# Kernel optimization log

Measured on AMD Instinct MI355X. Metric: run time of the kernel, lower is better.

## Reference

```python
import jax, jax.numpy as jnp
import numpy as np
from jax import lax

NUM_MASK_PARAMS = 67  # 66 weights (64 feat + 2 coord channels) + 1 bias
NUM_GEN_PARAMS = 134


def _coord_maps(h, w, dtype):
    yy = jnp.broadcast_to(jnp.linspace(-1.0, 1.0, h, dtype=dtype)[:, None], (h, w))
    xx = jnp.broadcast_to(jnp.linspace(-1.0, 1.0, w, dtype=dtype)[None, :], (h, w))
    return xx, yy


def _dynamic_head(x_cat, p):
    # x_cat: [66, H, W]; p: [num_ins, 67] -> [num_ins, H, W]
    w = p[:, :NUM_MASK_PARAMS - 1]
    b = p[:, NUM_MASK_PARAMS - 1]
    return jnp.einsum('ic,chw->ihw', w, x_cat) + b[:, None, None]


def setup_inputs() -> dict:
    key = jax.random.key(0)
    ks = jax.random.split(key, 10)
    C, HM, WM, HH, WH, MB, HID = 256, 272, 480, 136, 240, 64, 64
    rn = lambda k, s, sc=1.0: jax.random.normal(k, s, dtype=jnp.float32) * sc
    return {
        'out0': rn(ks[0], (1, C, HM, WM)),
        'out1': rn(ks[1], (1, C, HH, WH)),
        'hm_w': rn(ks[2], (1, C), 0.05),
        'hm_b': jnp.zeros((1,), jnp.float32),
        'params_w': rn(ks[3], (NUM_GEN_PARAMS, C), 0.05),
        'params_b': rn(ks[4], (NUM_GEN_PARAMS,), 0.05),
        'mb_w': rn(ks[5], (MB, C, 3, 3), 0.05),
        'mb_b': jnp.zeros((MB,), jnp.float32),
        'mlp_w1': rn(ks[6], (HM, HID), 0.05),
        'mlp_b1': jnp.zeros((HID,), jnp.float32),
        'mlp_w2': rn(ks[7], (HID, 2), 0.05),
        'mlp_b2': jnp.zeros((2,), jnp.float32),
        'num_ins': 4,
    }


def reference(out0, out1, hm_w, hm_b, params_w, params_b, mb_w, mb_b,
              mlp_w1, mlp_b1, mlp_w2, mlp_b2, num_ins):
    h_mask, w_mask = out0.shape[2], out0.shape[3]
    h_hm, w_hm = out1.shape[2], out1.shape[3]

    # ctnet head: 1x1 convs on the stride-16 feature
    hm = jnp.einsum('kc,bchw->bkhw', hm_w, out1) + hm_b[None, :, None, None]
    params = jnp.einsum('kc,bchw->bkhw', params_w, out1) + params_b[None, :, None, None]
    hm = jnp.clip(jax.nn.sigmoid(hm), 1e-4, 1.0 - 1e-4)  # [1,1,h_hm,w_hm]
    # [1,134,h,w] -> [h*w, 134]
    params_flat = jnp.transpose(params[0], (1, 2, 0)).reshape(-1, NUM_GEN_PARAMS)

    # 3x3 maxpool NMS (stride 1, pad 1), keep only local peaks
    hmax = lax.reduce_window(hm, -jnp.inf, lax.max, (1, 1, 3, 3), (1, 1, 1, 1),
                             [(0, 0), (0, 0), (1, 1), (1, 1)])
    keep = (hmax == hm).astype(hm.dtype)
    heat_nms = (hm * keep).reshape(-1)

    scores, inds = lax.top_k(heat_nms, num_ins)

    # mask branch: 3x3 conv + relu on the stride-8 feature
    mask_branch = lax.conv_general_dilated(out0, mb_w, (1, 1), 'SAME',
                                           dimension_numbers=('NCHW', 'OIHW', 'NCHW'))
    mask_branch = jax.nn.relu(mask_branch + mb_b[None, :, None, None])  # [1,64,H,W]

    xx, yy = _coord_maps(h_mask, w_mask, mask_branch.dtype)
    x_cat = jnp.concatenate([mask_branch[0], xx[None], yy[None]], axis=0)  # [66,H,W]

    gen_params = params_flat[inds]  # [num_ins, 134]
    masks0 = _dynamic_head(x_cat, gen_params[:, :NUM_MASK_PARAMS])   # [num_ins,H,W]
    regs0 = _dynamic_head(x_cat, gen_params[:, NUM_MASK_PARAMS:])    # [num_ins,H,W]

    # row-wise vertical-range MLP over h_mask
    feat_range = jnp.transpose(masks0, (0, 2, 1))  # [num_ins, w_mask, h_mask]
    h1 = jax.nn.relu(feat_range @ mlp_w1 + mlp_b1)
    feat_range = h1 @ mlp_w2 + mlp_b2  # [num_ins, w_mask, 2]

    return scores, inds, regs0, masks0, feat_range
```

## Files before the change

kernel.cpp:

```cpp
#include <hip/hip_runtime.h>
#include <math.h>
#include <limits.h>

#define C_IN 256
#define HM_H 136
#define HM_W 240
#define HM_N (HM_H * HM_W)
#define MB   64
#define MH   272
#define MW   480
#define MN   (MH * MW)
#define NP   134
#define NI   4
#define HID  64

#define REG_OFF   8
#define MASK_OFF  (8 + NI * MN)
#define FEAT_OFF  (8 + 2 * NI * MN)

#define WS_HM   0
#define WS_CV   HM_N
#define WS_CI   (HM_N + 512)
#define WS_GP   (2 * HM_N)
#define WS_INDS (2 * HM_N + NI * NP)
#define WS_WT_F 65824

typedef float  f32x4  __attribute__((ext_vector_type(4)));
typedef short  bf16x8 __attribute__((ext_vector_type(8)));

__device__ __forceinline__ unsigned short f2bf(float f) {
  unsigned int u = __float_as_uint(f);
  u += 0x7FFFu + ((u >> 16) & 1u);
  return (unsigned short)(u >> 16);
}
__device__ __forceinline__ float b2f(unsigned short h) {
  return __uint_as_float(((unsigned int)h) << 16);
}

__global__ void k_wprep(const float* __restrict__ mb_w, unsigned short* __restrict__ wt) {
  int idx = blockIdx.x * 256 + threadIdx.x;
  int j    = idx & 7;
  int lane = (idx >> 3) & 63;
  int nt   = (idx >> 9) & 3;
  int gt   = idx >> 11;
  int t    = gt % 9;
  int g    = gt / 9;
  int n = nt * 16 + (lane & 15);
  int c = g * 32 + (lane >> 4) * 8 + j;
  wt[idx] = f2bf(mb_w[(n * C_IN + c) * 9 + t]);
}

__global__ void k_hm(const float* __restrict__ out1, const float* __restrict__ hm_w,
                     const float* __restrict__ hm_b, float* __restrict__ ws_hm) {
  __shared__ float part[4][64];
  int b = blockIdx.x, t = threadIdx.x;
  int cg = t >> 6, pl = t & 63;
  int p = b * 64 + pl;
  float s = 0.f;
  #pragma unroll 16
  for (int c = 0; c < 64; ++c)
    s += hm_w[cg * 64 + c] * out1[(cg * 64 + c) * HM_N + p];
  part[cg][pl] = s;
  __syncthreads();
  if (t < 64) {
    float tot = part[0][t] + part[1][t] + part[2][t] + part[3][t] + hm_b[0];
    float sig = 1.f / (1.f + expf(-tot));
    sig = fminf(fmaxf(sig, 1e-4f), 1.f - 1e-4f);
    ws_hm[b * 64 + t] = sig;
  }
}

__device__ __forceinline__ bool better(float av, int ai, float bv, int bi) {
  return (av > bv) || (av == bv && ai < bi);
}

template<int NTHR>
__device__ void top4_tree(float* sv, int* si, int t) {
  for (int s = NTHR / 2; s >= 1; s >>= 1) {
    if (t < s) {
      float a[4], b[4]; int ai[4], bj[4];
      #pragma unroll
      for (int k = 0; k < 4; ++k) {
        a[k] = sv[t * 4 + k];        ai[k] = si[t * 4 + k];
        b[k] = sv[(t + s) * 4 + k];  bj[k] = si[(t + s) * 4 + k];
      }
      float ov[4]; int oi[4];
      int i = 0, j = 0;
      #pragma unroll
      for (int k = 0; k < 4; ++k) {
        if (better(a[i], ai[i], b[j], bj[j])) { ov[k] = a[i]; oi[k] = ai[i]; ++i; }
        else                                   { ov[k] = b[j]; oi[k] = bj[j]; ++j; }
      }
      #pragma unroll
      for (int k = 0; k < 4; ++k) { sv[t * 4 + k] = ov[k]; si[t * 4 + k] = oi[k]; }
    }
    __syncthreads();
  }
}

__global__ void k_nms_top(const float* __restrict__ ws_hm, float* __restrict__ candv,
                          int* __restrict__ candi) {
  __shared__ float sv[256 * 4];
  __shared__ int   si[256 * 4];
  int b = blockIdx.x, t = threadIdx.x;
  float v = -1.f; int idx = INT_MAX;
  if (t < 255) {
    int p = b * 255 + t;
    int y = p / HM_W, x = p - y * HM_W;
    float c = ws_hm[p], m = c;
    #pragma unroll
    for (int dy = -1; dy <= 1; ++dy)
      #pragma unroll
      for (int dx = -1; dx <= 1; ++dx) {
        int yy = y + dy, xx = x + dx;
        if (yy >= 0 && yy < HM_H && xx >= 0 && xx < HM_W)
          m = fmaxf(m, ws_hm[yy * HM_W + xx]);
      }
    v = (c == m) ? c : 0.f;
    idx = p;
  }
  sv[t * 4] = v; si[t * 4] = idx;
  #pragma unroll
  for (int k = 1; k < 4; ++k) { sv[t * 4 + k] = -1.f; si[t * 4 + k] = INT_MAX; }
  __syncthreads();
  top4_tree<256>(sv, si, t);
  if (t == 0) {
    #pragma unroll
    for (int k = 0; k < 4; ++k) { candv[b * 4 + k] = sv[k]; candi[b * 4 + k] = si[k]; }
  }
}

__global__ void k_topk_final(const float* __restrict__ candv, const int* __restrict__ candi,
                             int* __restrict__ ws_inds, float* __restrict__ d_out) {
  __shared__ float sv[128 * 4];
  __shared__ int   si[128 * 4];
  int t = threadIdx.x;
  #pragma unroll
  for (int k = 0; k < 4; ++k) { sv[t * 4 + k] = candv[t * 4 + k]; si[t * 4 + k] = candi[t * 4 + k]; }
  __syncthreads();
  top4_tree<128>(sv, si, t);
  if (t == 0) {
    #pragma unroll
    for (int k = 0; k < 4; ++k) {
      d_out[k]     = sv[k];
      d_out[4 + k] = (float)si[k];
      ws_inds[k]   = si[k];
    }
  }
}

__global__ void k_gen(const float* __restrict__ out1, const float* __restrict__ params_w,
                      const float* __restrict__ params_b, const int* __restrict__ ws_inds,
                      float* __restrict__ ws_gp) {
  __shared__ float col[C_IN];
  int i = blockIdx.x;
  int p = ws_inds[i];
  col[threadIdx.x] = out1[threadIdx.x * HM_N + p];
  __syncthreads();
  int j = threadIdx.x;
  if (j < NP) {
    float s = params_b[j];
    #pragma unroll 8
    for (int c = 0; c < C_IN; ++c) s += params_w[j * C_IN + c] * col[c];
    ws_gp[i * NP + j] = s;
  }
}

#define CS 40
#define RP 36
#define BUFU 14400

__global__ __launch_bounds__(256, 2) void k_conv_mfma(
    const float* __restrict__ out0, const unsigned short* __restrict__ wt,
    const float* __restrict__ mb_b, const float* __restrict__ ws_gp,
    float* __restrict__ d_out) {
  __shared__ unsigned short smem[2 * BUFU];

  int tid  = threadIdx.x;
  int lane = tid & 63;
  int w    = tid >> 6;
  int n15  = lane & 15;
  int kq   = lane >> 4;
  int gx0 = blockIdx.x * 32, gy0 = blockIdx.y * 8;

  int goff[25], lofs[25];
  unsigned int mld = 0, mst0 = 0, mst1 = 0;
  #pragma unroll
  for (int i = 0; i < 25; ++i) {
    int u = tid + 256 * i;
    int c   = u / 200;
    int rem = u - c * 200;
    int row = rem / 20;
    int q   = rem - row * 20;
    int iy  = gy0 + row - 1;
    int ixe = gx0 + 2 * q - 2;
    bool vld = (iy >= 0) && (iy < MH) && (ixe >= 0) && (ixe < MW);
    goff[i] = vld ? (c * MN + iy * MW + ixe) : 0;
    if (vld) mld |= (1u << i);
    int x0 = 2 * q - 1;
    lofs[i] = (row * RP + x0) * CS + c;
    if (x0 >= 0 && x0 < RP)     mst0 |= (1u << i);
    if (x0 + 1 < RP)            mst1 |= (1u << i);
  }

  int rrow[4], xbas[4];
  #pragma unroll
  for (int i = 0; i < 4; ++i) {
    int mt = w * 4 + i;
    rrow[i] = mt >> 1;
    xbas[i] = (mt & 1) * 16 + n15;
  }

  {
    float2 d[25];
    #pragma unroll
    for (int i = 0; i < 25; ++i) d[i] = *(const float2*)(out0 + goff[i]);
    #pragma unroll
    for (int i = 0; i < 25; ++i) {
      bool vl = (mld >> i) & 1;
      float a = vl ? d[i].x : 0.f, bb = vl ? d[i].y : 0.f;
      if ((mst0 >> i) & 1) smem[lofs[i]]      = f2bf(a);
      if ((mst1 >> i) & 1) smem[lofs[i] + CS] = f2bf(bb);
    }
  }
  __syncthreads();

  f32x4 acc[4][4];
  #pragma unroll
  for (int i = 0; i < 4; ++i)
    #pragma unroll
    for (int nt = 0; nt < 4; ++nt)
      acc[i][nt] = (f32x4){0.f, 0.f, 0.f, 0.f};

  #pragma unroll 1
  for (int g = 0; g < 8; ++g) {
    const unsigned short* cur = smem + (g & 1) * BUFU;
    unsigned short*       nxt = smem + ((g + 1) & 1) * BUFU;
    const float*          src = out0 + (g + 1) * (32 * MN);
    float2 d[25];

    if (g < 7) {
      #pragma unroll
      for (int i = 0; i < 13; ++i) d[i] = *(const float2*)(src + goff[i]);
    }
    #pragma unroll
    for (int t = 0; t < 4; ++t) {
      int ty = t / 3, tx = t - ty * 3;
      const unsigned short* wb = wt + (g * 9 + t) * 2048 + lane * 8;
      bf16x8 bfrag[4], afrag[4];
      #pragma unroll
      for (int nt = 0; nt < 4; ++nt) bfrag[nt] = *(const bf16x8*)(wb + nt * 512);
      #pragma unroll
      for (int i = 0; i < 4; ++i)
        afrag[i] = *(const bf16x8*)&cur[((rrow[i] + ty) * RP + xbas[i] + tx) * CS + kq * 8];
      #pragma unroll
      for (int i = 0; i < 4; ++i)
        #pragma unroll
        for (int nt = 0; nt < 4; ++nt)
          acc[i][nt] = __builtin_amdgcn_mfma_f32_16x16x32_bf16(afrag[i], bfrag[nt], acc[i][nt], 0, 0, 0);
    }
    if (g < 7) {
      #pragma unroll
      for (int i = 0; i < 13; ++i) {
        bool vl = (mld >> i) & 1;
        float a = vl ? d[i].x : 0.f, bb = vl ? d[i].y : 0.f;
        if ((mst0 >> i) & 1) nxt[lofs[i]]      = f2bf(a);
        if ((mst1 >> i) & 1) nxt[lofs[i] + CS] = f2bf(bb);
      }
      #pragma unroll
      for (int i = 13; i < 25; ++i) d[i] = *(const float2*)(src + goff[i]);
    }
    #pragma unroll
    for (int t = 4; t < 9; ++t) {
      int ty = t / 3, tx = t - ty * 3;
      const unsigned short* wb = wt + (g * 9 + t) * 2048 + lane * 8;
      bf16x8 bfrag[4], afrag[4];
      #pragma unroll
      for (int nt = 0; nt < 4; ++nt) bfrag[nt] = *(const bf16x8*)(wb + nt * 512);
      #pragma unroll
      for (int i = 0; i < 4; ++i)
        afrag[i] = *(const bf16x8*)&cur[((rrow[i] + ty) * RP + xbas[i] + tx) * CS + kq * 8];
      #pragma unroll
      for (int i = 0; i < 4; ++i)
        #pragma unroll
        for (int nt = 0; nt < 4; ++nt)
          acc[i][nt] = __builtin_amdgcn_mfma_f32_16x16x32_bf16(afrag[i], bfrag[nt], acc[i][nt], 0, 0, 0);
    }
    if (g < 7) {
      #pragma unroll
      for (int i = 13; i < 25; ++i) {
        bool vl = (mld >> i) & 1;
        float a = vl ? d[i].x : 0.f, bb = vl ? d[i].y : 0.f;
        if ((mst0 >> i) & 1) nxt[lofs[i]]      = f2bf(a);
        if ((mst1 >> i) & 1) nxt[lofs[i] + CS] = f2bf(bb);
      }
    }
    __syncthreads();
  }

  #define ES 66
  float bias[4];
  #pragma unroll
  for (int nt = 0; nt < 4; ++nt) bias[nt] = mb_b[nt * 16 + n15];
  #pragma unroll
  for (int i = 0; i < 4; ++i) {
    int mt = w * 4 + i;
    int pbase = (mt >> 1) * 32 + (mt & 1) * 16;
    #pragma unroll
    for (int nt = 0; nt < 4; ++nt)
      #pragma unroll
      for (int reg = 0; reg < 4; ++reg) {
        float vv = fmaxf(acc[i][nt][reg] + bias[nt], 0.f);
        smem[(pbase + kq * 4 + reg) * ES + nt * 16 + n15] = f2bf(vv);
      }
  }
  __syncthreads();

  int r = tid >> 5, xcol = tid & 31;
  int gy = gy0 + r, gx = gx0 + xcol;
  float xc = -1.f + (2.f / 479.f) * (float)gx;
  float yc = -1.f + (2.f / 271.f) * (float)gy;
  float mres[4] = {0.f, 0.f, 0.f, 0.f};
  float rres[4] = {0.f, 0.f, 0.f, 0.f};
  #pragma unroll 8
  for (int o = 0; o < MB; ++o) {
    float v = b2f(smem[tid * ES + o]);
    #pragma unroll
    for (int i = 0; i < 4; ++i) {
      mres[i] += ws_gp[i * NP + o] * v;
      rres[i] += ws_gp[i * NP + 67 + o] * v;
    }
  }
  int pix = gy * MW + gx;
  #pragma unroll
  for (int i = 0; i < 4; ++i) {
    const float* g = ws_gp + i * NP;
    d_out[MASK_OFF + i * MN + pix] = mres[i] + g[66]  + g[64]  * xc + g[65]  * yc;
    d_out[REG_OFF  + i * MN + pix] = rres[i] + g[133] + g[131] * xc + g[132] * yc;
  }
}

__global__ void k_mlp(const float* __restrict__ masks0, const float* __restrict__ w1,
                      const float* __restrict__ b1, const float* __restrict__ w2,
                      const float* __restrict__ b2, float* __restrict__ d_out) {
  int blk = blockIdx.x;
  int i = blk / MW;
  int w = blk - i * MW;
  int k = threadIdx.x;
  const float* mcol = masks0 + i * MN + w;
  float s = b1[k];
  for (int h = 0; h < MH; ++h) s += mcol[h * MW] * w1[h * HID + k];
  s = fmaxf(s, 0.f);
  float o0 = s * w2[k * 2 + 0];
  float o1 = s * w2[k * 2 + 1];
  #pragma unroll
  for (int off = 32; off >= 1; off >>= 1) {
    o0 += __shfl_down(o0, off);
    o1 += __shfl_down(o1, off);
  }
  if (k == 0) {
    d_out[FEAT_OFF + blk * 2 + 0] = o0 + b2[0];
    d_out[FEAT_OFF + blk * 2 + 1] = o1 + b2[1];
  }
}

extern "C" void kernel_launch(void* const* d_in, const int* in_sizes, int n_in,
                              void* d_out, int out_size, void* d_ws, size_t ws_size,
                              hipStream_t stream) {
  const float* out0     = (const float*)d_in[0];
  const float* out1     = (const float*)d_in[1];
  const float* hm_w     = (const float*)d_in[2];
  const float* hm_b     = (const float*)d_in[3];
  const float* params_w = (const float*)d_in[4];
  const float* params_b = (const float*)d_in[5];
  const float* mb_w     = (const float*)d_in[6];
  const float* mb_b     = (const float*)d_in[7];
  const float* mlp_w1   = (const float*)d_in[8];
  const float* mlp_b1   = (const float*)d_in[9];
  const float* mlp_w2   = (const float*)d_in[10];
  const float* mlp_b2   = (const float*)d_in[11];

  float* ws      = (float*)d_ws;
  float* ws_hm   = ws + WS_HM;
  float* candv   = ws + WS_CV;
  int*   candi   = (int*)(ws + WS_CI);
  float* ws_gp   = ws + WS_GP;
  int*   ws_inds = (int*)(ws + WS_INDS);
  unsigned short* ws_wt = (unsigned short*)(ws + WS_WT_F);
  float* out     = (float*)d_out;

  k_wprep<<<576, 256, 0, stream>>>(mb_w, ws_wt);
  k_hm  <<<510, 256, 0, stream>>>(out1, hm_w, hm_b, ws_hm);
  k_nms_top<<<128, 256, 0, stream>>>(ws_hm, candv, candi);
  k_topk_final<<<1, 128, 0, stream>>>(candv, candi, ws_inds, out);
  k_gen <<<NI, 256, 0, stream>>>(out1, params_w, params_b, ws_inds, ws_gp);
  dim3 gconv(MW / 32, MH / 8);
  k_conv_mfma<<<gconv, 256, 0, stream>>>(out0, ws_wt, mb_b, ws_gp, out);
  k_mlp <<<NI * MW, 64, 0, stream>>>(out + MASK_OFF, mlp_w1, mlp_b1, mlp_w2, mlp_b2, out);
}
```

Before: 356.9 us.

## Fuse small pre-kernels and single-buffer conv LDS with register-packed bf16 prefetch

New measurement: 409.5 us. 14.7% more time.

```diff
diff --git a/kernel.cpp b/kernel.cpp
--- a/kernel.cpp
+++ b/kernel.cpp
@@ -23,6 +23,7 @@
 #define WS_CI   (HM_N + 512)
 #define WS_GP   (2 * HM_N)
 #define WS_INDS (2 * HM_N + NI * NP)
+#define WS_CNT  (WS_INDS + 4)
 #define WS_WT_F 65824
 
 typedef float  f32x4  __attribute__((ext_vector_type(4)));
@@ -36,37 +37,44 @@
 __device__ __forceinline__ float b2f(unsigned short h) {
   return __uint_as_float(((unsigned int)h) << 16);
 }
-
-__global__ void k_wprep(const float* __restrict__ mb_w, unsigned short* __restrict__ wt) {
-  int idx = blockIdx.x * 256 + threadIdx.x;
-  int j    = idx & 7;
-  int lane = (idx >> 3) & 63;
-  int nt   = (idx >> 9) & 3;
-  int gt   = idx >> 11;
-  int t    = gt % 9;
-  int g    = gt / 9;
-  int n = nt * 16 + (lane & 15);
-  int c = g * 32 + (lane >> 4) * 8 + j;
-  wt[idx] = f2bf(mb_w[(n * C_IN + c) * 9 + t]);
-}
-
-__global__ void k_hm(const float* __restrict__ out1, const float* __restrict__ hm_w,
-                     const float* __restrict__ hm_b, float* __restrict__ ws_hm) {
+__device__ __forceinline__ unsigned int pk2(float lo, float hi) {
+  return (unsigned int)f2bf(lo) | ((unsigned int)f2bf(hi) << 16);
+}
+
+__global__ void k_pre(const float* __restrict__ mb_w, unsigned short* __restrict__ wt,
+                      const float* __restrict__ out1, const float* __restrict__ hm_w,
+                      const float* __restrict__ hm_b, float* __restrict__ ws_hm,
+                      unsigned int* __restrict__ cnt) {
   __shared__ float part[4][64];
   int b = blockIdx.x, t = threadIdx.x;
-  int cg = t >> 6, pl = t & 63;
-  int p = b * 64 + pl;
-  float s = 0.f;
-  #pragma unroll 16
-  for (int c = 0; c < 64; ++c)
-    s += hm_w[cg * 64 + c] * out1[(cg * 64 + c) * HM_N + p];
-  part[cg][pl] = s;
-  __syncthreads();
-  if (t < 64) {
-    float tot = part[0][t] + part[1][t] + part[2][t] + part[3][t] + hm_b[0];
-    float sig = 1.f / (1.f + expf(-tot));
-    sig = fminf(fmaxf(sig, 1e-4f), 1.f - 1e-4f);
-    ws_hm[b * 64 + t] = sig;
+  if (b == 0 && t == 0) *cnt = 0;
+  if (b < 576) {
+    int idx = b * 256 + t;
+    int j    = idx & 7;
+    int lane = (idx >> 3) & 63;
+    int nt   = (idx >> 9) & 3;
+    int gt   = idx >> 11;
+    int tp   = gt % 9;
+    int g    = gt / 9;
+    int n = nt * 16 + (lane & 15);
+    int c = g * 32 + (lane >> 4) * 8 + j;
+    wt[idx] = f2bf(mb_w[(n * C_IN + c) * 9 + tp]);
+  } else {
+    int bb = b - 576;
+    int cg = t >> 6, pl = t & 63;
+    int p = bb * 64 + pl;
+    float s = 0.f;
+    #pragma unroll 16
+    for (int c = 0; c < 64; ++c)
+      s += hm_w[cg * 64 + c] * out1[(cg * 64 + c) * HM_N + p];
+    part[cg][pl] = s;
+    __syncthreads();
+    if (t < 64) {
+      float tot = part[0][t] + part[1][t] + part[2][t] + part[3][t] + hm_b[0];
+      float sig = 1.f / (1.f + expf(-tot));
+      sig = fminf(fmaxf(sig, 1e-4f), 1.f - 1e-4f);
+      ws_hm[bb * 64 + t] = sig;
+    }
   }
 }
 
@@ -98,11 +106,17 @@
   }
 }
 
-__global__ void k_nms_top(const float* __restrict__ ws_hm, float* __restrict__ candv,
-                          int* __restrict__ candi) {
+__global__ void k_nms_merge(const float* __restrict__ ws_hm, float* __restrict__ candv,
+                            int* __restrict__ candi, unsigned int* __restrict__ cnt,
+                            const float* __restrict__ out1, const float* __restrict__ params_w,
+                            const float* __restrict__ params_b, int* __restrict__ ws_inds,
+                            float* __restrict__ ws_gp, float* __restrict__ d_out) {
   __shared__ float sv[256 * 4];
   __shared__ int   si[256 * 4];
+  __shared__ int   lastFlag;
+  __shared__ float col[4][C_IN];
   int b = blockIdx.x, t = threadIdx.x;
+
   float v = -1.f; int idx = INT_MAX;
   if (t < 255) {
     int p = b * 255 + t;
@@ -127,16 +141,18 @@
   if (t == 0) {
     #pragma unroll
     for (int k = 0; k < 4; ++k) { candv[b * 4 + k] = sv[k]; candi[b * 4 + k] = si[k]; }
-  }
-}
-
-__global__ void k_topk_final(const float* __restrict__ candv, const int* __restrict__ candi,
-                             int* __restrict__ ws_inds, float* __restrict__ d_out) {
-  __shared__ float sv[128 * 4];
-  __shared__ int   si[128 * 4];
-  int t = threadIdx.x;
-  #pragma unroll
-  for (int k = 0; k < 4; ++k) { sv[t * 4 + k] = candv[t * 4 + k]; si[t * 4 + k] = candi[t * 4 + k]; }
+    __threadfence();
+    unsigned int tk = atomicAdd(cnt, 1u);
+    lastFlag = (tk == 127u);
+  }
+  __syncthreads();
+  if (!lastFlag) return;
+  __threadfence();
+
+  if (t < 128) {
+    #pragma unroll
+    for (int k = 0; k < 4; ++k) { sv[t * 4 + k] = candv[t * 4 + k]; si[t * 4 + k] = candi[t * 4 + k]; }
+  }
   __syncthreads();
   top4_tree<128>(sv, si, t);
   if (t == 0) {
@@ -147,34 +163,33 @@
       ws_inds[k]   = si[k];
     }
   }
-}
-
-__global__ void k_gen(const float* __restrict__ out1, const float* __restrict__ params_w,
-                      const float* __restrict__ params_b, const int* __restrict__ ws_inds,
-                      float* __restrict__ ws_gp) {
-  __shared__ float col[C_IN];
-  int i = blockIdx.x;
-  int p = ws_inds[i];
-  col[threadIdx.x] = out1[threadIdx.x * HM_N + p];
-  __syncthreads();
-  int j = threadIdx.x;
-  if (j < NP) {
+  __syncthreads();
+
+  #pragma unroll
+  for (int i = 0; i < NI; ++i) col[i][t] = out1[t * HM_N + si[i]];
+  __syncthreads();
+  for (int o = t; o < NI * NP; o += 256) {
+    int i = o / NP, j = o - i * NP;
     float s = params_b[j];
     #pragma unroll 8
-    for (int c = 0; c < C_IN; ++c) s += params_w[j * C_IN + c] * col[c];
+    for (int c = 0; c < C_IN; ++c) s += params_w[j * C_IN + c] * col[i][c];
     ws_gp[i * NP + j] = s;
   }
 }
 
-#define CS 40
 #define RP 36
-#define BUFU 14400
-
-__global__ __launch_bounds__(256, 2) void k_conv_mfma(
+#define CSU 20
+#define NUNIT 2880
+#define UPT 12
+#define ES 66
+
+__global__ __launch_bounds__(256, 3) void k_conv_mfma(
     const float* __restrict__ out0, const unsigned short* __restrict__ wt,
     const float* __restrict__ mb_b, const float* __restrict__ ws_gp,
     float* __restrict__ d_out) {
-  __shared__ unsigned short smem[2 * BUFU];
+  __shared__ char smraw[33792] __attribute__((aligned(16)));
+  unsigned int*   lds32 = (unsigned int*)smraw;
+  unsigned short* lds16 = (unsigned short*)smraw;
 
   int tid  = threadIdx.x;
   int lane = tid & 63;
@@ -183,24 +198,25 @@
   int kq   = lane >> 4;
   int gx0 = blockIdx.x * 32, gy0 = blockIdx.y * 8;
 
-  int goff[25], lofs[25];
-  unsigned int mld = 0, mst0 = 0, mst1 = 0;
-  #pragma unroll
-  for (int i = 0; i < 25; ++i) {
+  int goff[UPT], lofs[UPT];
+  unsigned int vmask = 0, smask0 = 0, smask1 = 0;
+  #pragma unroll
+  for (int i = 0; i < UPT; ++i) {
     int u = tid + 256 * i;
-    int c   = u / 200;
-    int rem = u - c * 200;
-    int row = rem / 20;
-    int q   = rem - row * 20;
+    bool vu = (u < NUNIT);
+    int c2  = u / 180;
+    int rem = u - c2 * 180;
+    int row = rem / 18;
+    int q   = rem - row * 18;
     int iy  = gy0 + row - 1;
     int ixe = gx0 + 2 * q - 2;
-    bool vld = (iy >= 0) && (iy < MH) && (ixe >= 0) && (ixe < MW);
-    goff[i] = vld ? (c * MN + iy * MW + ixe) : 0;
-    if (vld) mld |= (1u << i);
+    bool vld = vu && iy >= 0 && iy < MH && ixe >= 0 && (ixe + 1) < MW;
+    goff[i] = vld ? (2 * c2 * MN + iy * MW + ixe) : 0;
+    if (vld) vmask |= (1u << i);
     int x0 = 2 * q - 1;
-    lofs[i] = (row * RP + x0) * CS + c;
-    if (x0 >= 0 && x0 < RP)     mst0 |= (1u << i);
-    if (x0 + 1 < RP)            mst1 |= (1u << i);
+    lofs[i] = (row * RP + x0) * CSU + c2;
+    if (vu && x0 >= 0) smask0 |= (1u << i);
+    if (vu)            smask1 |= (1u << i);
   }
 
   int rrow[4], xbas[4];
@@ -211,19 +227,21 @@
     xbas[i] = (mt & 1) * 16 + n15;
   }
 
+  unsigned int pkA[UPT], pkB[UPT];
   {
-    float2 d[25];
-    #pragma unroll
-    for (int i = 0; i < 25; ++i) d[i] = *(const float2*)(out0 + goff[i]);
-    #pragma unroll
-    for (int i = 0; i < 25; ++i) {
-      bool vl = (mld >> i) & 1;
-      float a = vl ? d[i].x : 0.f, bb = vl ? d[i].y : 0.f;
-      if ((mst0 >> i) & 1) smem[lofs[i]]      = f2bf(a);
-      if ((mst1 >> i) & 1) smem[lofs[i] + CS] = f2bf(bb);
-    }
-  }
-  __syncthreads();
+    float2 rA[UPT], rB[UPT];
+    #pragma unroll
+    for (int i = 0; i < UPT; ++i) {
+      rA[i] = *(const float2*)(out0 + goff[i]);
+      rB[i] = *(const float2*)(out0 + goff[i] + MN);
+    }
+    #pragma unroll
+    for (int i = 0; i < UPT; ++i) {
+      bool vl = (vmask >> i) & 1;
+      pkA[i] = vl ? pk2(rA[i].x, rB[i].x) : 0u;
+      pkB[i] = vl ? pk2(rA[i].y, rB[i].y) : 0u;
+    }
+  }
 
   f32x4 acc[4][4];
   #pragma unroll
@@ -234,14 +252,22 @@
 
   #pragma unroll 1
   for (int g = 0; g < 8; ++g) {
-    const unsigned short* cur = smem + (g & 1) * BUFU;
-    unsigned short*       nxt = smem + ((g + 1) & 1) * BUFU;
-    const float*          src = out0 + (g + 1) * (32 * MN);
-    float2 d[25];
-
+    __syncthreads();
+    #pragma unroll
+    for (int i = 0; i < UPT; ++i) {
+      if ((smask0 >> i) & 1) lds32[lofs[i]]       = pkA[i];
+      if ((smask1 >> i) & 1) lds32[lofs[i] + CSU] = pkB[i];
+    }
+    __syncthreads();
+
+    const float* src = out0 + (g + 1) * (32 * MN);
+    float2 rA[6], rB[6];
     if (g < 7) {
       #pragma unroll
-      for (int i = 0; i < 13; ++i) d[i] = *(const float2*)(src + goff[i]);
+      for (int i = 0; i < 6; ++i) {
+        rA[i] = *(const float2*)(src + goff[i]);
+        rB[i] = *(const float2*)(src + goff[i] + MN);
+      }
     }
     #pragma unroll
     for (int t = 0; t < 4; ++t) {
@@ -252,7 +278,7 @@
       for (int nt = 0; nt < 4; ++nt) bfrag[nt] = *(const bf16x8*)(wb + nt * 512);
       #pragma unroll
       for (int i = 0; i < 4; ++i)
-        afrag[i] = *(const bf16x8*)&cur[((rrow[i] + ty) * RP + xbas[i] + tx) * CS + kq * 8];
+        afrag[i] = *(const bf16x8*)&lds16[((rrow[i] + ty) * RP + xbas[i] + tx) * 40 + kq * 8];
       #pragma unroll
       for (int i = 0; i < 4; ++i)
         #pragma unroll
@@ -261,14 +287,16 @@
     }
     if (g < 7) {
       #pragma unroll
-      for (int i = 0; i < 13; ++i) {
-        bool vl = (mld >> i) & 1;
-        float a = vl ? d[i].x : 0.f, bb = vl ? d[i].y : 0.f;
-        if ((mst0 >> i) & 1) nxt[lofs[i]]      = f2bf(a);
-        if ((mst1 >> i) & 1) nxt[lofs[i] + CS] = f2bf(bb);
-      }
-      #pragma unroll
-      for (int i = 13; i < 25; ++i) d[i] = *(const float2*)(src + goff[i]);
+      for (int i = 0; i < 6; ++i) {
+        bool vl = (vmask >> i) & 1;
+        pkA[i] = vl ? pk2(rA[i].x, rB[i].x) : 0u;
+        pkB[i] = vl ? pk2(rA[i].y, rB[i].y) : 0u;
+      }
+      #pragma unroll
+      for (int i = 6; i < UPT; ++i) {
+        rA[i - 6] = *(const float2*)(src + goff[i]);
+        rB[i - 6] = *(const float2*)(src + goff[i] + MN);
+      }
     }
     #pragma unroll
     for (int t = 4; t < 9; ++t) {
@@ -279,7 +307,7 @@
       for (int nt = 0; nt < 4; ++nt) bfrag[nt] = *(const bf16x8*)(wb + nt * 512);
       #pragma unroll
       for (int i = 0; i < 4; ++i)
-        afrag[i] = *(const bf16x8*)&cur[((rrow[i] + ty) * RP + xbas[i] + tx) * CS + kq * 8];
+        afrag[i] = *(const bf16x8*)&lds16[((rrow[i] + ty) * RP + xbas[i] + tx) * 40 + kq * 8];
       #pragma unroll
       for (int i = 0; i < 4; ++i)
         #pragma unroll
@@ -288,20 +316,18 @@
     }
     if (g < 7) {
       #pragma unroll
-      for (int i = 13; i < 25; ++i) {
-        bool vl = (mld >> i) & 1;
-        float a = vl ? d[i].x : 0.f, bb = vl ? d[i].y : 0.f;
-        if ((mst0 >> i) & 1) nxt[lofs[i]]      = f2bf(a);
-        if ((mst1 >> i) & 1) nxt[lofs[i] + CS] = f2bf(bb);
-      }
-    }
-    __syncthreads();
-  }
-
-  #define ES 66
+      for (int i = 6; i < UPT; ++i) {
+        bool vl = (vmask >> i) & 1;
+        pkA[i] = vl ? pk2(rA[i - 6].x, rB[i - 6].x) : 0u;
+        pkB[i] = vl ? pk2(rA[i - 6].y, rB[i - 6].y) : 0u;
+      }
+    }
+  }
+
   float bias[4];
   #pragma unroll
   for (int nt = 0; nt < 4; ++nt) bias[nt] = mb_b[nt * 16 + n15];
+  __syncthreads();
   #pragma unroll
   for (int i = 0; i < 4; ++i) {
     int mt = w * 4 + i;
@@ -311,7 +337,7 @@
       #pragma unroll
       for (int reg = 0; reg < 4; ++reg) {
         float vv = fmaxf(acc[i][nt][reg] + bias[nt], 0.f);
-        smem[(pbase + kq * 4 + reg) * ES + nt * 16 + n15] = f2bf(vv);
+        lds16[(pbase + kq * 4 + reg) * ES + nt * 16 + n15] = f2bf(vv);
       }
   }
   __syncthreads();
@@ -324,7 +350,7 @@
   float rres[4] = {0.f, 0.f, 0.f, 0.f};
   #pragma unroll 8
   for (int o = 0; o < MB; ++o) {
-    float v = b2f(smem[tid * ES + o]);
+    float v = b2f(lds16[tid * ES + o]);
     #pragma unroll
     for (int i = 0; i < 4; ++i) {
       mres[i] += ws_gp[i * NP + o] * v;
@@ -386,15 +412,14 @@
   int*   candi   = (int*)(ws + WS_CI);
   float* ws_gp   = ws + WS_GP;
   int*   ws_inds = (int*)(ws + WS_INDS);
+  unsigned int* cnt = (unsigned int*)(ws + WS_CNT);
   unsigned short* ws_wt = (unsigned short*)(ws + WS_WT_F);
   float* out     = (float*)d_out;
 
-  k_wprep<<<576, 256, 0, stream>>>(mb_w, ws_wt);
-  k_hm  <<<510, 256, 0, stream>>>(out1, hm_w, hm_b, ws_hm);
-  k_nms_top<<<128, 256, 0, stream>>>(ws_hm, candv, candi);
-  k_topk_final<<<1, 128, 0, stream>>>(candv, candi, ws_inds, out);
-  k_gen <<<NI, 256, 0, stream>>>(out1, params_w, params_b, ws_inds, ws_gp);
+  k_pre<<<1086, 256, 0, stream>>>(mb_w, ws_wt, out1, hm_w, hm_b, ws_hm, cnt);
+  k_nms_merge<<<128, 256, 0, stream>>>(ws_hm, candv, candi, cnt, out1,
+                                       params_w, params_b, ws_inds, ws_gp, out);
   dim3 gconv(MW / 32, MH / 8);
   k_conv_mfma<<<gconv, 256, 0, stream>>>(out0, ws_wt, mb_b, ws_gp, out);
-  k_mlp <<<NI * MW, 64, 0, stream>>>(out + MASK_OFF, mlp_w1, mlp_b1, mlp_w2, mlp_b2, out);
-}
+  k_mlp<<<NI * MW, 64, 0, stream>>>(out + MASK_OFF, mlp_w1, mlp_b1, mlp_w2, mlp_b2, out);
+}
```
